# Kernel optimization log

Hardware: AMD Instinct MI355X
Metric: run time of the kernel (lower is better)

Reference implementation:

```python
import jax, jax.numpy as jnp
import numpy as np

B, H, W, C, NH, WS = 4, 128, 128, 128, 4, 8
N = WS * WS
HD = C // NH
SCALE = HD ** -0.5
MLP_H = 4 * C


def _rel_index():
    coords = np.stack(np.meshgrid(np.arange(WS), np.arange(WS), indexing='ij'))
    flat = coords.reshape(2, -1)
    rel = (flat[:, :, None] - flat[:, None, :]).transpose(1, 2, 0).astype(np.int64)
    rel[..., 0] += WS - 1
    rel[..., 1] += WS - 1
    rel[..., 0] *= 2 * WS - 1
    return jnp.asarray(rel.sum(-1))  # (N, N)

REL_IDX = _rel_index()


def layer_norm(x, w, b):
    m = jnp.mean(x, -1, keepdims=True)
    v = jnp.mean((x - m) ** 2, -1, keepdims=True)
    return (x - m) * jax.lax.rsqrt(v + 1e-5) * w + b


def window_partition(x):  # (B, H*W, C) -> (B*nW, N, C)
    t = x.reshape(B, H // WS, WS, W // WS, WS, C).transpose(0, 1, 3, 2, 4, 5)
    return t.reshape(-1, N, C)


def window_reverse(wins):  # (B*nW, N, C) -> (B, H*W, C)
    t = wins.reshape(B, H // WS, W // WS, WS, WS, C).transpose(0, 1, 3, 2, 4, 5)
    return t.reshape(B, H * W, C)


def setup_inputs():
    key = jax.random.key(0)
    ks = jax.random.split(key, 8)
    rn = lambda k, s: jax.random.normal(k, s, jnp.float32) * 0.02
    return {
        'x': jax.random.normal(ks[0], (B, H * W, C), jnp.float32),
        'd': jax.random.normal(ks[1], (B, H * W, C), jnp.float32),
        'rpb_table': rn(ks[2], ((2 * WS - 1) ** 2, NH)),
        'norm1_w': jnp.ones((C,), jnp.float32), 'norm1_b': jnp.zeros((C,), jnp.float32),
        'norm2_w': jnp.ones((C,), jnp.float32), 'norm2_b': jnp.zeros((C,), jnp.float32),
        'qkv1_w': rn(ks[3], (4 * C, C)), 'qkv1_b': jnp.zeros((4 * C,), jnp.float32),
        'proj_w': rn(ks[4], (C, C)), 'proj_b': jnp.zeros((C,), jnp.float32),
        'fc1_w': rn(ks[5], (MLP_H, C)), 'fc1_b': jnp.zeros((MLP_H,), jnp.float32),
        'fc2_w': rn(ks[6], (C, MLP_H)), 'fc2_b': jnp.zeros((C,), jnp.float32),
    }


def _attn_core(xw, dw, rpb_table, qkv1_w, qkv1_b, proj_w, proj_b):
    def qkv(t):
        q = (t @ qkv1_w.T + qkv1_b).reshape(-1, N, 4, NH, HD)
        return jnp.moveaxis(q, 2, 0).transpose(0, 1, 3, 2, 4)  # (4, B_, NH, N, HD)

    q_r, k_r, v_r, q_rd = qkv(xw)
    q_d, k_d, v_d, q_dr = qkv(dw)
    bias = rpb_table[REL_IDX].transpose(2, 0, 1)  # (NH, N, N)
    sm = jax.nn.softmax
    dot = lambda q, k: jnp.einsum('bhnd,bhmd->bhnm', q * SCALE, k)
    attn = sm(dot(q_r, k_r) + bias[None])      # bias only on r-branch (as in torch)
    attn_rd = sm(dot(q_dr, k_r))
    attn_d = sm(dot(q_d, k_d))
    attn_dr = sm(dot(q_rd, k_d))
    av = lambda a, v: jnp.einsum('bhnm,bhmd->bhnd', a, v).transpose(0, 2, 1, 3).reshape(-1, N, C)
    x_out = av(attn, v_r) + av(attn_rd, v_r)
    d_out = av(attn_dr, v_d) + av(attn_d, v_d)
    return x_out @ proj_w.T + proj_b, d_out @ proj_w.T + proj_b


def reference(x, d, rpb_table, norm1_w, norm1_b, norm2_w, norm2_b, qkv1_w, qkv1_b, proj_w, proj_b, fc1_w, fc1_b, fc2_w, fc2_b):
    xw = window_partition(layer_norm(x, norm1_w, norm1_b))
    dw = window_partition(layer_norm(d, norm1_w, norm1_b))
    xa, da = _attn_core(xw, dw, rpb_table, qkv1_w, qkv1_b, proj_w, proj_b)
    x = x + window_reverse(xa)
    d = d + window_reverse(da)
    mlp = lambda t: jax.nn.gelu(t @ fc1_w.T + fc1_b, approximate=False) @ fc2_w.T + fc2_b
    x = x + mlp(layer_norm(x, norm2_w, norm2_b))
    d = d + mlp(layer_norm(d, norm2_w, norm2_b))
    return x, d
```

## Files before the change

kernel.cpp:

```cpp
#include <hip/hip_runtime.h>
#include <hip/hip_bf16.h>
#include <math.h>

typedef short bf16x8 __attribute__((ext_vector_type(8)));
typedef float f32x4 __attribute__((ext_vector_type(4)));

#define QKSCALE_L2E 0.25505402227437564f
#define LOG2E 1.4426950408889634f

__device__ __forceinline__ unsigned short f2bf(float f) {
  __hip_bfloat16 h = __float2bfloat16(f);
  return *reinterpret_cast<unsigned short*>(&h);
}
__device__ __forceinline__ unsigned int pk2(float lo, float hi) {
  __hip_bfloat162 h = __float22bfloat162_rn(make_float2(lo, hi));
  return *reinterpret_cast<unsigned int*>(&h);
}
__device__ __forceinline__ bf16x8 pack8(const float* g) {
  union { unsigned int u[4]; bf16x8 v; } t;
  t.u[0] = pk2(g[0], g[1]); t.u[1] = pk2(g[2], g[3]);
  t.u[2] = pk2(g[4], g[5]); t.u[3] = pk2(g[6], g[7]);
  return t.v;
}

__device__ __forceinline__ bf16x8 ldsv(const unsigned short* base, int row, int strideHalfs, int kHalf, int swzMask) {
  int byte = row * strideHalfs * 2 + kHalf * 2;
  byte ^= (row & swzMask) << 4;
  return *(const bf16x8*)((const char*)base + byte);
}
__device__ __forceinline__ void ldss(unsigned short* base, int row, int strideHalfs, int col, int swzMask, unsigned short v) {
  int byte = row * strideHalfs * 2 + col * 2;
  byte ^= (row & swzMask) << 4;
  *(unsigned short*)((char*)base + byte) = v;
}
__device__ __forceinline__ void ldst32(unsigned short* base, int row, int strideHalfs, int colHalf, int swzMask, unsigned int v) {
  int byte = row * strideHalfs * 2 + colHalf * 2;
  byte ^= (row & swzMask) << 4;
  *(unsigned int*)((char*)base + byte) = v;
}
__device__ __forceinline__ void ldst64(unsigned short* base, int row, int strideHalfs, int colHalf, int swzMask, unsigned int lo, unsigned int hi) {
  int byte = row * strideHalfs * 2 + colHalf * 2;
  byte ^= (row & swzMask) << 4;
  uint2 val; val.x = lo; val.y = hi;
  *(uint2*)((char*)base + byte) = val;
}
__device__ __forceinline__ void ldst128(unsigned short* base, int row, int strideHalfs, int colHalf, int swzMask, bf16x8 v) {
  int byte = row * strideHalfs * 2 + colHalf * 2;
  byte ^= (row & swzMask) << 4;
  *(bf16x8*)((char*)base + byte) = v;
}

__global__ void prep_kernel(
    const float* __restrict__ qkv1_w, const float* __restrict__ qkv1_b,
    const float* __restrict__ proj_w, const float* __restrict__ fc1_w,
    const float* __restrict__ fc2_w,  const float* __restrict__ rpb,
    unsigned short* __restrict__ Wqkvf, unsigned short* __restrict__ Wprojf,
    unsigned short* __restrict__ Wfc1f, unsigned short* __restrict__ Wfc2f,
    float* __restrict__ bqkv, float* __restrict__ biasmat)
{
  int i = blockIdx.x * 256 + threadIdx.x;
  if (i < 65536) {
    int j = i & 7, lane = (i >> 3) & 63, kk = (i >> 9) & 3;
    int sub16 = (i >> 11) & 1, h = (i >> 12) & 3, comp = i >> 14;
    int row = comp * 128 + h * 32 + sub16 * 16 + (lane & 15);
    int col = kk * 32 + (lane >> 4) * 8 + j;
    float sc = (comp == 0 || comp == 3) ? QKSCALE_L2E : 1.f;
    Wqkvf[i] = f2bf(qkv1_w[row * 128 + col] * sc);
  }
  int o = i - 65536;
  if (o >= 0 && o < 16384) {
    int j = o & 7, lane = (o >> 3) & 63, kk = (o >> 9) & 3, nf = o >> 11;
    int row = nf * 16 + (lane & 15);
    int cp = kk * 32 + (lane >> 4) * 8 + j;
    int H = cp >> 5, q = cp & 31, a = q >> 1, b = q & 1;
    Wprojf[o] = f2bf(proj_w[row * 128 + H * 32 + 16 * b + a]);
  }
  o -= 16384;
  if (o >= 0 && o < 65536) {
    int j = o & 7, lane = (o >> 3) & 63, kk = (o >> 9) & 3, n16 = o >> 11;
    int row = n16 * 16 + (lane & 15);
    int cp = kk * 32 + (lane >> 4) * 8 + j;
    Wfc1f[o] = f2bf(fc1_w[row * 128 + 16 * (cp & 7) + (cp >> 3)]);
  }
  o -= 65536;
  if (o >= 0 && o < 65536) {
    int j = o & 7, lane = (o >> 3) & 63, kk = (o >> 9) & 15, n8 = o >> 13;
    int row = n8 * 16 + (lane & 15);
    int m = kk * 32 + (lane >> 4) * 8 + j;
    int mm = m & 127;
    Wfc2f[o] = f2bf(fc2_w[row * 512 + (m >> 7) * 128 + 16 * (mm & 7) + (mm >> 3)]);
  }
  o -= 65536;
  if (o >= 0 && o < 512) {
    int comp = o >> 7;
    bqkv[o] = qkv1_b[o] * ((comp == 0 || comp == 3) ? QKSCALE_L2E : 1.f);
  }
  o -= 512;
  if (o >= 0 && o < 16384) {
    int hh = o >> 12, n = (o >> 6) & 63, m = o & 63;
    int di = (n >> 3) - (m >> 3) + 7, dj = (n & 7) - (m & 7) + 7;
    biasmat[o] = rpb[(di * 15 + dj) * 4 + hh] * LOG2E;
  }
}

__global__ void __launch_bounds__(256) ln1_kernel(
    const float* __restrict__ x_in, const float* __restrict__ d_in_,
    const float* __restrict__ n1w, const float* __restrict__ n1b,
    unsigned short* __restrict__ xg)
{
  const int s = blockIdx.x >> 10;
  const int row0 = (blockIdx.x & 1023) * 64;
  const int t = threadIdx.x >> 2, q4 = threadIdx.x & 3;
  const int grow = row0 + t;
  const int b2 = grow >> 14, rem = grow & 16383;
  const int gy = rem >> 7, gx = rem & 127;
  const int win = b2 * 256 + (gy >> 3) * 16 + (gx >> 3);
  const int tok = (gy & 7) * 8 + (gx & 7);
  const float* src = (s ? d_in_ : x_in) + (size_t)grow * 128 + q4 * 32;
  float v[32];
  float sum = 0.f, ss = 0.f;
#pragma unroll
  for (int i = 0; i < 8; ++i) {
    float4 f = ((const float4*)src)[i];
    v[i * 4 + 0] = f.x; v[i * 4 + 1] = f.y; v[i * 4 + 2] = f.z; v[i * 4 + 3] = f.w;
    sum += f.x + f.y + f.z + f.w;
    ss += f.x * f.x + f.y * f.y + f.z * f.z + f.w * f.w;
  }
  sum += __shfl_xor(sum, 1); sum += __shfl_xor(sum, 2);
  ss  += __shfl_xor(ss, 1);  ss  += __shfl_xor(ss, 2);
  float mean = sum * (1.f / 128.f);
  float var = ss * (1.f / 128.f) - mean * mean;
  float rs = rsqrtf(var + 1e-5f);
  unsigned short* base = xg + ((size_t)(s * 1024 + win)) * 8192
                         + ((tok >> 4) * 4 + q4) * 512 + (tok & 15) * 8;
#pragma unroll
  for (int i = 0; i < 4; ++i) {
    float g[8];
#pragma unroll
    for (int jj = 0; jj < 8; ++jj) {
      int c = q4 * 32 + i * 8 + jj;
      g[jj] = (v[i * 8 + jj] - mean) * rs * n1w[c] + n1b[c];
    }
    *(bf16x8*)(base + i * 128) = pack8(g);
  }
}

__global__ void __launch_bounds__(256, 4) attn_kernel(
    const unsigned short* __restrict__ xg,
    const unsigned short* __restrict__ Wqkvf, const float* __restrict__ bqkv,
    const float* __restrict__ biasmat,
    unsigned short* __restrict__ aout)
{
  __shared__ unsigned short smem[2][10240];

  const int tid = threadIdx.x, wid = tid >> 6, lane = tid & 63;
  const int l4 = lane >> 4, l15 = lane & 15;
  const int win = blockIdx.x >> 2, h = blockIdx.x & 3;
  const f32x4 fzero = {0.f, 0.f, 0.f, 0.f};

  bf16x8 aF[2][4];
#pragma unroll
  for (int s = 0; s < 2; ++s) {
    const unsigned short* xw = xg + ((size_t)(s * 1024 + win)) * 8192;
#pragma unroll
    for (int kk = 0; kk < 4; ++kk)
      aF[s][kk] = *(const bf16x8*)(xw + (wid * 4 + kk) * 512 + lane * 8);
  }

  {
    f32x4 acc[2][8];
#pragma unroll
    for (int s = 0; s < 2; ++s)
#pragma unroll
      for (int n = 0; n < 8; ++n) acc[s][n] = fzero;
#pragma unroll
    for (int kk = 0; kk < 4; ++kk)
#pragma unroll
      for (int nf = 0; nf < 8; ++nf) {
        const int frag = (((nf >> 1) * 4 + h) * 2 + (nf & 1)) * 4 + kk;
        bf16x8 bb = *(const bf16x8*)(Wqkvf + frag * 512 + lane * 8);
        acc[0][nf] = __builtin_amdgcn_mfma_f32_16x16x32_bf16(aF[0][kk], bb, acc[0][nf], 0, 0, 0);
        acc[1][nf] = __builtin_amdgcn_mfma_f32_16x16x32_bf16(aF[1][kk], bb, acc[1][nf], 0, 0, 0);
      }
    float bv[8];
#pragma unroll
    for (int nf = 0; nf < 8; ++nf) bv[nf] = bqkv[(nf >> 1) * 128 + h * 32 + (nf & 1) * 16 + l15];
#pragma unroll
    for (int s = 0; s < 2; ++s)
#pragma unroll
      for (int r = 0; r < 4; ++r) {
        const int tw = wid * 16 + l4 * 4 + r;
        ldst32(smem[s] + 0,    tw, 32, 2 * l15, 3, pk2(acc[s][0][r] + bv[0], acc[s][1][r] + bv[1]));
        ldst32(smem[s] + 4096, tw, 32, 2 * l15, 3, pk2(acc[s][2][r] + bv[2], acc[s][3][r] + bv[3]));
        ldst32(smem[s] + 2048, tw, 32, 2 * l15, 3, pk2(acc[s][6][r] + bv[6], acc[s][7][r] + bv[7]));
        const int vc = 16 * l4 + 4 * r + wid;
        ldss(smem[s] + 8192, l15,      64, vc, 7, f2bf(acc[s][4][r] + bv[4]));
        ldss(smem[s] + 8192, 16 + l15, 64, vc, 7, f2bf(acc[s][5][r] + bv[5]));
      }
  }
  __syncthreads();

  const int s = wid >> 1, kind = wid & 1;
  bf16x8 aR[4], kR[4];
  {
    const unsigned short* Ab = kind ? (smem[1 - s] + 2048) : (smem[s] + 0);
    const unsigned short* Kb = smem[s] + 4096;
#pragma unroll
    for (int mf = 0; mf < 4; ++mf) aR[mf] = ldsv(Ab, mf * 16 + l15, 32, l4 * 8, 3);
#pragma unroll
    for (int nf = 0; nf < 4; ++nf) kR[nf] = ldsv(Kb, nf * 16 + l15, 32, l4 * 8, 3);
  }
  __syncthreads();

  f32x4 sc[4][4];
#pragma unroll
  for (int mf = 0; mf < 4; ++mf)
#pragma unroll
    for (int nf = 0; nf < 4; ++nf) sc[mf][nf] = fzero;
#pragma unroll
  for (int mf = 0; mf < 4; ++mf)
#pragma unroll
    for (int nf = 0; nf < 4; ++nf)
      sc[mf][nf] = __builtin_amdgcn_mfma_f32_16x16x32_bf16(aR[mf], kR[nf], sc[mf][nf], 0, 0, 0);

  if (s == 0 && kind == 0) {
#pragma unroll
    for (int mf = 0; mf < 4; ++mf)
#pragma unroll
      for (int nf = 0; nf < 4; ++nf)
#pragma unroll
        for (int r = 0; r < 4; ++r) {
          int row = mf * 16 + l4 * 4 + r, col = nf * 16 + l15;
          sc[mf][nf][r] += biasmat[(h * 64 + row) * 64 + col];
        }
  }
#pragma unroll
  for (int mf = 0; mf < 4; ++mf) {
    float M = sc[mf][0][0];
#pragma unroll
    for (int nf = 0; nf < 4; ++nf)
#pragma unroll
      for (int r = 0; r < 4; ++r) M = fmaxf(M, sc[mf][nf][r]);
    M = fmaxf(M, __shfl_xor(M, 1));
    M = fmaxf(M, __shfl_xor(M, 2));
    M = fmaxf(M, __shfl_xor(M, 4));
    M = fmaxf(M, __shfl_xor(M, 8));
#pragma unroll
    for (int r = 0; r < 4; ++r) {
      float e0 = __builtin_amdgcn_exp2f(sc[mf][0][r] - M);
      float e1 = __builtin_amdgcn_exp2f(sc[mf][1][r] - M);
      float e2 = __builtin_amdgcn_exp2f(sc[mf][2][r] - M);
      float e3 = __builtin_amdgcn_exp2f(sc[mf][3][r] - M);
      float sm = e0 + e1 + e2 + e3;
      sm += __shfl_xor(sm, 1); sm += __shfl_xor(sm, 2);
      sm += __shfl_xor(sm, 4); sm += __shfl_xor(sm, 8);
      float inv = __builtin_amdgcn_rcpf(sm);
      sc[mf][0][r] = e0 * inv; sc[mf][1][r] = e1 * inv;
      sc[mf][2][r] = e2 * inv; sc[mf][3][r] = e3 * inv;
    }
  }
  {
    unsigned short* Ptgt = smem[s] + (kind ? 4096 : 0);
#pragma unroll
    for (int mf = 0; mf < 4; ++mf)
#pragma unroll
      for (int r = 0; r < 4; ++r)
        ldst64(Ptgt, mf * 16 + l4 * 4 + r, 64, 4 * l15, 7,
               pk2(sc[mf][0][r], sc[mf][1][r]), pk2(sc[mf][2][r], sc[mf][3][r]));
  }
  __syncthreads();

  {
    const unsigned short* Vt = smem[s] + 8192;
    bf16x8 vR[2][2];
#pragma unroll
    for (int kk = 0; kk < 2; ++kk)
#pragma unroll
      for (int nf = 0; nf < 2; ++nf) vR[kk][nf] = ldsv(Vt, nf * 16 + l15, 64, kk * 32 + l4 * 8, 7);
    f32x4 pv[2][2];
    pv[0][0] = fzero; pv[0][1] = fzero; pv[1][0] = fzero; pv[1][1] = fzero;
#pragma unroll
    for (int pb_i = 0; pb_i < 2; ++pb_i) {
      const unsigned short* Pbuf = smem[s] + pb_i * 4096;
#pragma unroll
      for (int kk = 0; kk < 2; ++kk) {
        bf16x8 pa0 = ldsv(Pbuf, kind * 32 + l15, 64, kk * 32 + l4 * 8, 7);
        bf16x8 pa1 = ldsv(Pbuf, kind * 32 + 16 + l15, 64, kk * 32 + l4 * 8, 7);
#pragma unroll
        for (int nf = 0; nf < 2; ++nf) {
          pv[0][nf] = __builtin_amdgcn_mfma_f32_16x16x32_bf16(pa0, vR[kk][nf], pv[0][nf], 0, 0, 0);
          pv[1][nf] = __builtin_amdgcn_mfma_f32_16x16x32_bf16(pa1, vR[kk][nf], pv[1][nf], 0, 0, 0);
        }
      }
    }
#pragma unroll
    for (int mf = 0; mf < 2; ++mf)
#pragma unroll
      for (int r = 0; r < 4; ++r) {
        int tw = kind * 32 + mf * 16 + l4 * 4 + r;
        *(unsigned int*)(aout + ((size_t)s * 65536 + (size_t)win * 64 + tw) * 128 + h * 32 + 2 * l15) =
            pk2(pv[mf][0][r], pv[mf][1][r]);
      }
  }
}

__global__ void __launch_bounds__(256, 4) proj_kernel(
    const unsigned short* __restrict__ aout, const unsigned short* __restrict__ Wprojf,
    const float* __restrict__ projb,
    const float* __restrict__ x_in, const float* __restrict__ d_in_,
    const float* __restrict__ n2w, const float* __restrict__ n2b,
    float* __restrict__ out, unsigned short* __restrict__ xn2)
{
  const int tid = threadIdx.x, wid = tid >> 6, lane = tid & 63;
  const int l4 = lane >> 4, l15 = lane & 15;
  const int s = blockIdx.x >> 9, blk = blockIdx.x & 511;
  const int row0 = blk * 128 + wid * 32;
  const unsigned short* A = aout + (size_t)s * 65536 * 128;
  const f32x4 fzero = {0.f, 0.f, 0.f, 0.f};

  bf16x8 aF[2][4];
#pragma unroll
  for (int mf = 0; mf < 2; ++mf)
#pragma unroll
    for (int kk = 0; kk < 4; ++kk)
      aF[mf][kk] = *(const bf16x8*)(A + (size_t)(row0 + mf * 16 + l15) * 128 + kk * 32 + l4 * 8);

  f32x4 acc[2][8];
#pragma unroll
  for (int mf = 0; mf < 2; ++mf)
#pragma unroll
    for (int nf = 0; nf < 8; ++nf) acc[mf][nf] = fzero;
#pragma unroll
  for (int kk = 0; kk < 4; ++kk)
#pragma unroll
    for (int nf = 0; nf < 8; ++nf) {
      bf16x8 bb = *(const bf16x8*)(Wprojf + (nf * 4 + kk) * 512 + lane * 8);
      acc[0][nf] = __builtin_amdgcn_mfma_f32_16x16x32_bf16(aF[0][kk], bb, acc[0][nf], 0, 0, 0);
      acc[1][nf] = __builtin_amdgcn_mfma_f32_16x16x32_bf16(aF[1][kk], bb, acc[1][nf], 0, 0, 0);
    }

  float pbv[8], w2v[8], b2v[8];
#pragma unroll
  for (int nf = 0; nf < 8; ++nf) {
    int col = nf * 16 + l15;
    pbv[nf] = projb[col]; w2v[nf] = n2w[col]; b2v[nf] = n2b[col];
  }
  const float* resid = s ? d_in_ : x_in;
  float* dst = out + (size_t)s * 8388608;
#pragma unroll
  for (int mf = 0; mf < 2; ++mf)
#pragma unroll
    for (int r = 0; r < 4; ++r) {
      int t = row0 + mf * 16 + l4 * 4 + r;
      int w2 = t >> 6, tk = t & 63;
      int b2 = w2 >> 8, hb = (w2 >> 4) & 15, wb = w2 & 15;
      int grow = b2 * 16384 + hb * 1024 + (tk >> 3) * 128 + wb * 8 + (tk & 7);
      float v[8];
      float sum = 0.f, ssq = 0.f;
#pragma unroll
      for (int nf = 0; nf < 8; ++nf) {
        size_t off = (size_t)grow * 128 + nf * 16 + l15;
        float val = acc[mf][nf][r] + pbv[nf] + resid[off];
        v[nf] = val; sum += val; ssq += val * val;
        dst[off] = val;
      }
      sum += __shfl_xor(sum, 1); sum += __shfl_xor(sum, 2);
      sum += __shfl_xor(sum, 4); sum += __shfl_xor(sum, 8);
      ssq += __shfl_xor(ssq, 1); ssq += __shfl_xor(ssq, 2);
      ssq += __shfl_xor(ssq, 4); ssq += __shfl_xor(ssq, 8);
      float mean = sum * (1.f / 128.f);
      float var = ssq * (1.f / 128.f) - mean * mean;
      float rs = rsqrtf(var + 1e-5f);
      float g[8];
#pragma unroll
      for (int nf = 0; nf < 8; ++nf) g[nf] = (v[nf] - mean) * rs * w2v[nf] + b2v[nf];
      size_t fidx = ((size_t)s * 4096 + (grow >> 4)) * 4 + (l15 >> 2);
      *(bf16x8*)(xn2 + fidx * 512 + ((l15 & 3) * 16 + (grow & 15)) * 8) = pack8(g);
    }
}

__global__ void __launch_bounds__(256, 4) mlp_kernel(
    const unsigned short* __restrict__ xn2,
    const unsigned short* __restrict__ Wfc1f, const float* __restrict__ fc1b,
    const unsigned short* __restrict__ Wfc2f, const float* __restrict__ fc2b,
    float* __restrict__ out)
{
  __shared__ unsigned short hbuf[32 * 512];
  const int tid = threadIdx.x, wid = tid >> 6, lane = tid & 63;
  const int l4 = lane >> 4, l15 = lane & 15;
  const size_t rbase = (size_t)blockIdx.x * 32;
  const f32x4 fzero = {0.f, 0.f, 0.f, 0.f};

  {
    bf16x8 aF[2][4];
#pragma unroll
    for (int mf = 0; mf < 2; ++mf)
#pragma unroll
      for (int kk = 0; kk < 4; ++kk)
        aF[mf][kk] = *(const bf16x8*)(xn2 + (((size_t)blockIdx.x * 2 + mf) * 4 + kk) * 512 + lane * 8);
    f32x4 acc[2][8];
#pragma unroll
    for (int mf = 0; mf < 2; ++mf)
#pragma unroll
      for (int nf = 0; nf < 8; ++nf) acc[mf][nf] = fzero;
#pragma unroll
    for (int kk = 0; kk < 4; ++kk)
#pragma unroll
      for (int nf = 0; nf < 8; ++nf) {
        bf16x8 bb = *(const bf16x8*)(Wfc1f + (((wid * 8 + nf) * 4) + kk) * 512 + lane * 8);
        acc[0][nf] = __builtin_amdgcn_mfma_f32_16x16x32_bf16(aF[0][kk], bb, acc[0][nf], 0, 0, 0);
        acc[1][nf] = __builtin_amdgcn_mfma_f32_16x16x32_bf16(aF[1][kk], bb, acc[1][nf], 0, 0, 0);
      }
    float b1v[8];
#pragma unroll
    for (int nf = 0; nf < 8; ++nf) b1v[nf] = fc1b[wid * 128 + nf * 16 + l15];
#pragma unroll
    for (int mf = 0; mf < 2; ++mf)
#pragma unroll
      for (int r = 0; r < 4; ++r) {
        float g[8];
#pragma unroll
        for (int nf = 0; nf < 8; ++nf) {
          float vv = acc[mf][nf][r] + b1v[nf];
          float x2 = vv * vv;
          float u2 = vv * fmaf(-0.10294455f, x2, -2.3022078f);
          float e = __builtin_amdgcn_exp2f(u2);
          g[nf] = vv * __builtin_amdgcn_rcpf(1.f + e);
        }
        ldst128(hbuf, mf * 16 + l4 * 4 + r, 512, wid * 128 + l15 * 8, 7, pack8(g));
      }
  }
  __syncthreads();
  {
    f32x4 a2[2][2];
    a2[0][0] = fzero; a2[0][1] = fzero; a2[1][0] = fzero; a2[1][1] = fzero;
#pragma unroll
    for (int kk = 0; kk < 16; ++kk) {
      bf16x8 h0 = ldsv(hbuf, l15, 512, kk * 32 + l4 * 8, 7);
      bf16x8 h1 = ldsv(hbuf, 16 + l15, 512, kk * 32 + l4 * 8, 7);
#pragma unroll
      for (int nf = 0; nf < 2; ++nf) {
        bf16x8 bb = *(const bf16x8*)(Wfc2f + (((wid * 2 + nf) * 16) + kk) * 512 + lane * 8);
        a2[0][nf] = __builtin_amdgcn_mfma_f32_16x16x32_bf16(h0, bb, a2[0][nf], 0, 0, 0);
        a2[1][nf] = __builtin_amdgcn_mfma_f32_16x16x32_bf16(h1, bb, a2[1][nf], 0, 0, 0);
      }
    }
#pragma unroll
    for (int mf = 0; mf < 2; ++mf)
#pragma unroll
      for (int nf = 0; nf < 2; ++nf) {
        int col = wid * 32 + nf * 16 + l15;
        float bias = fc2b[col];
#pragma unroll
        for (int r = 0; r < 4; ++r) {
          int row = mf * 16 + l4 * 4 + r;
          size_t off = (rbase + row) * 128 + col;
          out[off] = a2[mf][nf][r] + bias + out[off];
        }
      }
  }
}

extern "C" void kernel_launch(void* const* d_in, const int* in_sizes, int n_in,
                              void* d_out, int out_size, void* d_ws, size_t ws_size,
                              hipStream_t stream) {
  const float* x    = (const float*)d_in[0];
  const float* dd   = (const float*)d_in[1];
  const float* rpb  = (const float*)d_in[2];
  const float* n1w  = (const float*)d_in[3];
  const float* n1b  = (const float*)d_in[4];
  const float* n2w  = (const float*)d_in[5];
  const float* n2b  = (const float*)d_in[6];
  const float* qkvw = (const float*)d_in[7];
  const float* qkvb = (const float*)d_in[8];
  const float* pw   = (const float*)d_in[9];
  const float* pb   = (const float*)d_in[10];
  const float* f1w  = (const float*)d_in[11];
  const float* f1b  = (const float*)d_in[12];
  const float* f2w  = (const float*)d_in[13];
  const float* f2b  = (const float*)d_in[14];
  float* out = (float*)d_out;
  char* ws = (char*)d_ws;
  unsigned short* Wqkvf  = (unsigned short*)(ws);
  unsigned short* Wprojf = (unsigned short*)(ws + 131072);
  unsigned short* Wfc1f  = (unsigned short*)(ws + 163840);
  unsigned short* Wfc2f  = (unsigned short*)(ws + 294912);
  float* bqkv            = (float*)(ws + 425984);
  float* biasmat         = (float*)(ws + 428032);
  unsigned short* aout   = (unsigned short*)(ws + 524288);
  unsigned short* xn2    = (unsigned short*)(ws + 524288 + 33554432);
  unsigned short* xg     = (unsigned short*)d_out;

  prep_kernel<<<dim3(899), dim3(256), 0, stream>>>(qkvw, qkvb, pw, f1w, f2w, rpb,
                                                   Wqkvf, Wprojf, Wfc1f, Wfc2f, bqkv, biasmat);
  ln1_kernel<<<dim3(2048), dim3(256), 0, stream>>>(x, dd, n1w, n1b, xg);
  attn_kernel<<<dim3(4096), dim3(256), 0, stream>>>(xg, Wqkvf, bqkv, biasmat, aout);
  proj_kernel<<<dim3(1024), dim3(256), 0, stream>>>(aout, Wprojf, pb, x, dd, n2w, n2b, out, xn2);
  mlp_kernel<<<dim3(4096), dim3(256), 0, stream>>>(xn2, Wfc1f, f1b, Wfc2f, f2b, out);
}
```

Baseline: 230.6 us.

## Make MLP kernel persistent with fc1/fc2 weights held in registers

The MLP kernel now launches 256 blocks of 512 threads. Each block loads its wave's slice of the fc1 and fc2 weight fragments into registers once, then loops over 16 tiles of 32 tokens. Before, 4096 blocks each reloaded the weights from global memory. Using 8 waves splits the hidden dimension into 64-column slices, and the fc2 weight permutation in prep is redone to match the new hidden-column layout in LDS. The cost is much higher register pressure, 256 blocks for the GPU's CUs, and a barrier per tile, with no overlap between tiles.

```diff
diff --git a/kernel.cpp b/kernel.cpp
--- a/kernel.cpp
+++ b/kernel.cpp
@@ -43,11 +43,6 @@
   byte ^= (row & swzMask) << 4;
   uint2 val; val.x = lo; val.y = hi;
   *(uint2*)((char*)base + byte) = val;
-}
-__device__ __forceinline__ void ldst128(unsigned short* base, int row, int strideHalfs, int colHalf, int swzMask, bf16x8 v) {
-  int byte = row * strideHalfs * 2 + colHalf * 2;
-  byte ^= (row & swzMask) << 4;
-  *(bf16x8*)((char*)base + byte) = v;
 }
 
 __global__ void prep_kernel(
@@ -87,8 +82,8 @@
     int j = o & 7, lane = (o >> 3) & 63, kk = (o >> 9) & 15, n8 = o >> 13;
     int row = n8 * 16 + (lane & 15);
     int m = kk * 32 + (lane >> 4) * 8 + j;
-    int mm = m & 127;
-    Wfc2f[o] = f2bf(fc2_w[row * 512 + (m >> 7) * 128 + 16 * (mm & 7) + (mm >> 3)]);
+    int src = (m >> 6) * 64 + 16 * (m & 3) + ((m >> 2) & 15);
+    Wfc2f[o] = f2bf(fc2_w[row * 512 + src]);
   }
   o -= 65536;
   if (o >= 0 && o < 512) {
@@ -379,7 +374,7 @@
     }
 }
 
-__global__ void __launch_bounds__(256, 4) mlp_kernel(
+__global__ void __launch_bounds__(512, 2) mlp_kernel(
     const unsigned short* __restrict__ xn2,
     const unsigned short* __restrict__ Wfc1f, const float* __restrict__ fc1b,
     const unsigned short* __restrict__ Wfc2f, const float* __restrict__ fc2b,
@@ -388,75 +383,73 @@
   __shared__ unsigned short hbuf[32 * 512];
   const int tid = threadIdx.x, wid = tid >> 6, lane = tid & 63;
   const int l4 = lane >> 4, l15 = lane & 15;
-  const size_t rbase = (size_t)blockIdx.x * 32;
   const f32x4 fzero = {0.f, 0.f, 0.f, 0.f};
 
-  {
-    bf16x8 aF[2][4];
+  bf16x8 wf1[16], wf2[16];
+#pragma unroll
+  for (int q = 0; q < 16; ++q)
+    wf1[q] = *(const bf16x8*)(Wfc1f + (size_t)((wid * 4 + (q >> 2)) * 4 + (q & 3)) * 512 + lane * 8);
+#pragma unroll
+  for (int kk = 0; kk < 16; ++kk)
+    wf2[kk] = *(const bf16x8*)(Wfc2f + (size_t)(wid * 16 + kk) * 512 + lane * 8);
+
+  float b1v[4];
+#pragma unroll
+  for (int nf = 0; nf < 4; ++nf) b1v[nf] = fc1b[wid * 64 + nf * 16 + l15];
+  const float b2c = fc2b[wid * 16 + l15];
+  const int ocol = wid * 16 + l15;
+
+  const size_t tokbase = (size_t)blockIdx.x * 512;
+
+  for (int it = 0; it < 16; ++it) {
+    if (it) __syncthreads();
+    const size_t tb = tokbase + it * 32;
+    f32x4 acc[2][4];
 #pragma unroll
     for (int mf = 0; mf < 2; ++mf)
 #pragma unroll
-      for (int kk = 0; kk < 4; ++kk)
-        aF[mf][kk] = *(const bf16x8*)(xn2 + (((size_t)blockIdx.x * 2 + mf) * 4 + kk) * 512 + lane * 8);
-    f32x4 acc[2][8];
+      for (int nf = 0; nf < 4; ++nf) acc[mf][nf] = fzero;
 #pragma unroll
     for (int mf = 0; mf < 2; ++mf)
 #pragma unroll
-      for (int nf = 0; nf < 8; ++nf) acc[mf][nf] = fzero;
-#pragma unroll
-    for (int kk = 0; kk < 4; ++kk)
-#pragma unroll
-      for (int nf = 0; nf < 8; ++nf) {
-        bf16x8 bb = *(const bf16x8*)(Wfc1f + (((wid * 8 + nf) * 4) + kk) * 512 + lane * 8);
-        acc[0][nf] = __builtin_amdgcn_mfma_f32_16x16x32_bf16(aF[0][kk], bb, acc[0][nf], 0, 0, 0);
-        acc[1][nf] = __builtin_amdgcn_mfma_f32_16x16x32_bf16(aF[1][kk], bb, acc[1][nf], 0, 0, 0);
-      }
-    float b1v[8];
-#pragma unroll
-    for (int nf = 0; nf < 8; ++nf) b1v[nf] = fc1b[wid * 128 + nf * 16 + l15];
+      for (int kk = 0; kk < 4; ++kk) {
+        bf16x8 a = *(const bf16x8*)(xn2 + (((tb >> 4) + mf) * 4 + kk) * 512 + lane * 8);
+#pragma unroll
+        for (int nf = 0; nf < 4; ++nf)
+          acc[mf][nf] = __builtin_amdgcn_mfma_f32_16x16x32_bf16(a, wf1[nf * 4 + kk], acc[mf][nf], 0, 0, 0);
+      }
 #pragma unroll
     for (int mf = 0; mf < 2; ++mf)
 #pragma unroll
       for (int r = 0; r < 4; ++r) {
-        float g[8];
-#pragma unroll
-        for (int nf = 0; nf < 8; ++nf) {
+        float g[4];
+#pragma unroll
+        for (int nf = 0; nf < 4; ++nf) {
           float vv = acc[mf][nf][r] + b1v[nf];
           float x2 = vv * vv;
           float u2 = vv * fmaf(-0.10294455f, x2, -2.3022078f);
           float e = __builtin_amdgcn_exp2f(u2);
           g[nf] = vv * __builtin_amdgcn_rcpf(1.f + e);
         }
-        ldst128(hbuf, mf * 16 + l4 * 4 + r, 512, wid * 128 + l15 * 8, 7, pack8(g));
-      }
-  }
-  __syncthreads();
-  {
-    f32x4 a2[2][2];
-    a2[0][0] = fzero; a2[0][1] = fzero; a2[1][0] = fzero; a2[1][1] = fzero;
+        ldst64(hbuf, mf * 16 + l4 * 4 + r, 512, wid * 64 + l15 * 4, 7,
+               pk2(g[0], g[1]), pk2(g[2], g[3]));
+      }
+    __syncthreads();
+    f32x4 a2[2];
+    a2[0] = fzero; a2[1] = fzero;
 #pragma unroll
     for (int kk = 0; kk < 16; ++kk) {
       bf16x8 h0 = ldsv(hbuf, l15, 512, kk * 32 + l4 * 8, 7);
       bf16x8 h1 = ldsv(hbuf, 16 + l15, 512, kk * 32 + l4 * 8, 7);
-#pragma unroll
-      for (int nf = 0; nf < 2; ++nf) {
-        bf16x8 bb = *(const bf16x8*)(Wfc2f + (((wid * 2 + nf) * 16) + kk) * 512 + lane * 8);
-        a2[0][nf] = __builtin_amdgcn_mfma_f32_16x16x32_bf16(h0, bb, a2[0][nf], 0, 0, 0);
-        a2[1][nf] = __builtin_amdgcn_mfma_f32_16x16x32_bf16(h1, bb, a2[1][nf], 0, 0, 0);
-      }
+      a2[0] = __builtin_amdgcn_mfma_f32_16x16x32_bf16(h0, wf2[kk], a2[0], 0, 0, 0);
+      a2[1] = __builtin_amdgcn_mfma_f32_16x16x32_bf16(h1, wf2[kk], a2[1], 0, 0, 0);
     }
 #pragma unroll
     for (int mf = 0; mf < 2; ++mf)
 #pragma unroll
-      for (int nf = 0; nf < 2; ++nf) {
-        int col = wid * 32 + nf * 16 + l15;
-        float bias = fc2b[col];
-#pragma unroll
-        for (int r = 0; r < 4; ++r) {
-          int row = mf * 16 + l4 * 4 + r;
-          size_t off = (rbase + row) * 128 + col;
-          out[off] = a2[mf][nf][r] + bias + out[off];
-        }
+      for (int r = 0; r < 4; ++r) {
+        size_t off = (tb + mf * 16 + l4 * 4 + r) * 128 + ocol;
+        out[off] = a2[mf][r] + b2c + out[off];
       }
   }
 }
@@ -496,5 +489,5 @@
   ln1_kernel<<<dim3(2048), dim3(256), 0, stream>>>(x, dd, n1w, n1b, xg);
   attn_kernel<<<dim3(4096), dim3(256), 0, stream>>>(xg, Wqkvf, bqkv, biasmat, aout);
   proj_kernel<<<dim3(1024), dim3(256), 0, stream>>>(aout, Wprojf, pb, x, dd, n2w, n2b, out, xn2);
-  mlp_kernel<<<dim3(4096), dim3(256), 0, stream>>>(xn2, Wfc1f, f1b, Wfc2f, f2b, out);
-}
+  mlp_kernel<<<dim3(256), dim3(512), 0, stream>>>(xn2, Wfc1f, f1b, Wfc2f, f2b, out);
+}
```

Result: faster. 212.3 us (-7.9%).
